# Optimization experiments

Measured on AMD Instinct MI355X. Metric: run time of the kernel, lower is better.

Reference implementation:

```python
import jax, jax.numpy as jnp
import numpy as np

B, T, W, D = 2, 64, 32, 512
H = 8                      # n_heads
N = 64                     # d_state
EXPAND = 2
DIN = EXPAND * D           # 1024 d_inner
R = -(-D // 16)            # dt_rank = ceil(d_model/16) = 32
K = 4                      # d_conv (mamba default)


def setup_inputs():
    key = jax.random.key(0)
    ks = jax.random.split(key, 20)
    s = 0.02
    inp = {
        'x': jax.random.normal(ks[0], (B, T, W, D), jnp.float32),
        'wq': jax.random.normal(ks[1], (D, D), jnp.float32) * s,
        'bq': jnp.zeros((D,), jnp.float32),
        'wk': jax.random.normal(ks[2], (D, D), jnp.float32) * s,
        'bk': jnp.zeros((D,), jnp.float32),
        'wv': jax.random.normal(ks[3], (D, D), jnp.float32) * s,
        'bv': jnp.zeros((D,), jnp.float32),
        'wo': jax.random.normal(ks[4], (D, D), jnp.float32) * s,
        'bo': jnp.zeros((D,), jnp.float32),
        'in_proj_w': jax.random.normal(ks[5], (2 * DIN, D), jnp.float32) * s,
        'conv_w': jax.random.normal(ks[6], (DIN, 1, K), jnp.float32) * 0.2,
        'conv_b': jnp.zeros((DIN,), jnp.float32),
        'x_proj_w': jax.random.normal(ks[7], (R + 2 * N, DIN), jnp.float32) * s,
        'dt_proj_w': jax.random.normal(ks[8], (DIN, R), jnp.float32) * 0.1,
        'dt_proj_b': jnp.full((DIN,), -4.6, jnp.float32),  # ~softplus^-1(0.01)
        'A_log': jnp.log(jnp.broadcast_to(jnp.arange(1, N + 1, dtype=jnp.float32), (DIN, N))),
        'D_param': jnp.ones((DIN,), jnp.float32),
        'out_proj_w': jax.random.normal(ks[9], (D, DIN), jnp.float32) * s,
        'ln_w': jnp.ones((D,), jnp.float32),
        'ln_b': jnp.zeros((D,), jnp.float32),
    }
    return inp


def _attention(xf, wq, bq, wk, bk, wv, bv, wo, bo):
    b, L, d = xf.shape
    e = d // H
    q = (xf @ wq.T + bq).reshape(b, L, H, e)
    k = (xf @ wk.T + bk).reshape(b, L, H, e)
    v = (xf @ wv.T + bv).reshape(b, L, H, e)
    scale = 1.0 / jnp.sqrt(jnp.float32(e))
    scores = jnp.einsum('blhe,bshe->bhls', q, k) * scale
    causal = jnp.tril(jnp.ones((L, L), bool))
    scores = jnp.where(causal, scores, jnp.finfo(scores.dtype).min)
    attn = jax.nn.softmax(scores, axis=-1)  # dropout off (eval mode)
    out = jnp.einsum('bhls,bshe->blhe', attn, v).reshape(b, L, d)
    return out @ wo.T + bo


def _mamba(xf, in_proj_w, conv_w, conv_b, x_proj_w, dt_proj_w, dt_proj_b,
           A_log, D_param, out_proj_w):
    b, L, d = xf.shape
    xz = xf @ in_proj_w.T                 # (B,L,2*DIN)
    x_in, z = jnp.split(xz, 2, axis=-1)
    # causal depthwise conv1d over L
    xc = jnp.transpose(x_in, (0, 2, 1))   # (B,DIN,L)
    xc = jax.lax.conv_general_dilated(
        xc, conv_w, window_strides=(1,), padding=[(K - 1, 0)],
        feature_group_count=DIN, dimension_numbers=('NCH', 'OIH', 'NCH'))
    xc = xc + conv_b[None, :, None]
    u = jax.nn.silu(jnp.transpose(xc, (0, 2, 1)))   # (B,L,DIN)
    dbc = u @ x_proj_w.T                             # (B,L,R+2N)
    dt, Bm, Cm = dbc[..., :R], dbc[..., R:R + N], dbc[..., R + N:]
    dt = jax.nn.softplus(dt @ dt_proj_w.T + dt_proj_b)  # (B,L,DIN)
    A = -jnp.exp(A_log)                                 # (DIN,N)

    def step(h, t):
        dt_t, B_t, C_t, u_t = t  # (b,DIN),(b,N),(b,N),(b,DIN)
        dA = jnp.exp(dt_t[..., None] * A)                       # (b,DIN,N)
        h = dA * h + (dt_t * u_t)[..., None] * B_t[:, None, :]  # (b,DIN,N)
        y = jnp.einsum('bdn,bn->bd', h, C_t)
        return h, y

    h0 = jnp.zeros((b, DIN, N), xf.dtype)
    xs = (jnp.swapaxes(dt, 0, 1), jnp.swapaxes(Bm, 0, 1),
          jnp.swapaxes(Cm, 0, 1), jnp.swapaxes(u, 0, 1))
    _, ys = jax.lax.scan(step, h0, xs)
    y = jnp.swapaxes(ys, 0, 1) + u * D_param   # (B,L,DIN)
    y = y * jax.nn.silu(z)
    return y @ out_proj_w.T


def reference(x, wq, bq, wk, bk, wv, bv, wo, bo, in_proj_w, conv_w, conv_b,
              x_proj_w, dt_proj_w, dt_proj_b, A_log, D_param, out_proj_w,
              ln_w, ln_b):
    b, t, w, d = x.shape
    L = t * w
    xf = x.reshape(b, L, d)
    x_attn = _attention(xf, wq, bq, wk, bk, wv, bv, wo, bo).reshape(b, t, w, d)
    x_mamba = _mamba(xf, in_proj_w, conv_w, conv_b, x_proj_w, dt_proj_w,
                     dt_proj_b, A_log, D_param, out_proj_w).reshape(b, t, w, d)
    h = x + x_attn + x_mamba
    mu = jnp.mean(h, axis=-1, keepdims=True)
    var = jnp.mean(jnp.square(h - mu), axis=-1, keepdims=True)
    return (h - mu) * jax.lax.rsqrt(var + 1e-5) * ln_w + ln_b
```

## Files before the change

kernel.cpp:

```cpp
#include <hip/hip_runtime.h>

typedef __attribute__((ext_vector_type(4))) float f32x4;
typedef __attribute__((ext_vector_type(8))) short short8;
typedef __attribute__((ext_vector_type(2))) unsigned uint2e;

#define DEV static __device__ __forceinline__

DEV ushort f2b(float f) {
  union { float f; unsigned u; } v; v.f = f;
  unsigned r = v.u + 0x7FFF + ((v.u >> 16) & 1);
  return (ushort)(r >> 16);
}
DEV unsigned pack_bf2(float lo, float hi) {
  return (unsigned)f2b(lo) | ((unsigned)f2b(hi) << 16);
}
DEV float bflo(unsigned p) { return __uint_as_float(p << 16); }
DEV float bfhi(unsigned p) { return __uint_as_float(p & 0xFFFF0000u); }
DEV float b2f(ushort u) { return __uint_as_float((unsigned)u << 16); }

DEV float fexp2(float x) { float r; asm("v_exp_f32 %0, %1" : "=v"(r) : "v"(x)); return r; }

DEV float xor32_add_lo(float s) {
  uint2e r = __builtin_amdgcn_permlane32_swap(__float_as_uint(s), __float_as_uint(s), false, false);
  return s + __uint_as_float(r.x);
}

#define QP(x, ctrl) __int_as_float(__builtin_amdgcn_update_dpp(0, __float_as_int(x), (ctrl), 0xf, 0xf, false))
#define SWZ(x, off) __int_as_float(__builtin_amdgcn_ds_swizzle(__float_as_int(x), (off)))
#define DPP_ADD(x, ctrl, rmask) \
  ((x) + __int_as_float(__builtin_amdgcn_update_dpp(0, __float_as_int(x), (ctrl), (rmask), 0xf, false)))

#define LOG2E 1.44269504f

#define BB    2
#define LL    2048
#define DD    512
#define HH    8
#define EE    64
#define DIN   1024
#define NS    64
#define RR    32
#define BL    4096
#define NCH   16
#define TC    128
#define NC    1536
#define NQ    3584
#define XOFF  1536
#define ZOFF  2560
#define MFMA(a,b,c) __builtin_amdgcn_mfma_f32_16x16x32_bf16((a),(b),(c),0,0,0)

struct CvtJobs {
  const float* src[7];
  ushort*      dst[7];
  int          n[7];
};

__global__ __launch_bounds__(256) void cvt_multi(CvtJobs j) {
  int job = blockIdx.y;
  const float* s = j.src[job];
  ushort* d = j.dst[job];
  int n = j.n[job];
  for (int i = blockIdx.x * 256 + threadIdx.x; i < n; i += gridDim.x * 256)
    d[i] = f2b(s[i]);
}

__global__ __launch_bounds__(256) void pack_wcomb(
    const float* __restrict__ wo, const float* __restrict__ opw,
    const float* __restrict__ bq, const float* __restrict__ bk,
    const float* __restrict__ bv, ushort* __restrict__ wc,
    float* __restrict__ bqi)
{
  int i = blockIdx.x * 256 + threadIdx.x;
  if (i < NQ)
    bqi[i] = (i < DD) ? bq[i] : (i < 2 * DD) ? bk[i - DD] : (i < NC) ? bv[i - 2 * DD] : 0.f;
  if (i >= DD * NC) return;
  int n = i / NC, c = i - n * NC;
  float v = (c < DD) ? wo[n * DD + c] : opw[n * DIN + (c - DD)];
  wc[i] = f2b(v);
}

__global__ __launch_bounds__(256) void gemm_bt(
    const ushort* __restrict__ A, const ushort* __restrict__ W,
    const float* __restrict__ bias, float* __restrict__ outF,
    ushort* __restrict__ outB, int M, int N, int K, int act)
{
  __shared__ ushort As[64][40];
  __shared__ ushort Ws[64][40];
  int m0 = blockIdx.y * 64, n0 = blockIdx.x * 64;
  int tid = threadIdx.x, l = tid & 63, w = tid >> 6;
  int wm = (w >> 1) * 32, wn = (w & 1) * 32;
  int lr = l & 15, kl = (l >> 4) * 8;
  int srow = tid >> 2, sk = (tid & 3) * 8;
  f32x4 acc[2][2] = {};

  for (int k0 = 0; k0 < K; k0 += 32) {
    uint4 av = *(const uint4*)&A[(size_t)(m0 + srow) * K + k0 + sk];
    uint4 wv;
    if (n0 + srow < N) wv = *(const uint4*)&W[(size_t)(n0 + srow) * K + k0 + sk];
    else { wv.x = 0; wv.y = 0; wv.z = 0; wv.w = 0; }
    *(uint4*)&As[srow][sk] = av;
    *(uint4*)&Ws[srow][sk] = wv;
    __syncthreads();
    short8 a0 = *(const short8*)&As[wm + lr][kl];
    short8 a1 = *(const short8*)&As[wm + 16 + lr][kl];
    short8 b0 = *(const short8*)&Ws[wn + lr][kl];
    short8 b1 = *(const short8*)&Ws[wn + 16 + lr][kl];
    acc[0][0] = MFMA(a0, b0, acc[0][0]);
    acc[0][1] = MFMA(a0, b1, acc[0][1]);
    acc[1][0] = MFMA(a1, b0, acc[1][0]);
    acc[1][1] = MFMA(a1, b1, acc[1][1]);
    __syncthreads();
  }

  #pragma unroll
  for (int mi = 0; mi < 2; mi++)
    #pragma unroll
    for (int ni = 0; ni < 2; ni++) {
      int rbase = m0 + wm + mi * 16 + ((l >> 4) << 2);
      int col = n0 + wn + ni * 16 + lr;
      if (col < N) {
        float bval = bias ? bias[col] : 0.f;
        #pragma unroll
        for (int r = 0; r < 4; r++) {
          float v = acc[mi][ni][r] + bval;
          if (act == 1) v = (v > 20.f) ? v : log1pf(__expf(v));
          size_t o = (size_t)(rbase + r) * N + col;
          if (outF) outF[o] = v;
          if (outB) outB[o] = f2b(v);
        }
      }
    }
}

__global__ __launch_bounds__(256) void gemm128(
    const ushort* __restrict__ A, const ushort* __restrict__ W,
    const float* __restrict__ bias, float* __restrict__ outF,
    ushort* __restrict__ outB, int M, int N, int K)
{
  __shared__ ushort As[128][40];
  __shared__ ushort Ws[128][40];
  int tid = threadIdx.x, l = tid & 63, w = tid >> 6;
  int m0 = blockIdx.y * 128, n0 = blockIdx.x * 128;
  int wm = (w >> 1) * 64, wn = (w & 1) * 64;
  int lr = l & 15, kl = (l >> 4) * 8;
  int srow = tid >> 1, sk = (tid & 1) * 16;
  f32x4 acc[4][4] = {};

  const ushort* Ap = A + (size_t)(m0 + srow) * K + sk;
  const ushort* Wp = W + (size_t)(n0 + srow) * K + sk;

  for (int k0 = 0; k0 < K; k0 += 32) {
    uint4 a0 = *(const uint4*)(Ap);
    uint4 a1 = *(const uint4*)(Ap + 8);
    uint4 b0 = *(const uint4*)(Wp);
    uint4 b1 = *(const uint4*)(Wp + 8);
    __syncthreads();
    *(uint4*)&As[srow][sk]     = a0;
    *(uint4*)&As[srow][sk + 8] = a1;
    *(uint4*)&Ws[srow][sk]     = b0;
    *(uint4*)&Ws[srow][sk + 8] = b1;
    __syncthreads();
    short8 af[4], bf[4];
    #pragma unroll
    for (int mi = 0; mi < 4; mi++) af[mi] = *(const short8*)&As[wm + mi * 16 + lr][kl];
    #pragma unroll
    for (int ni = 0; ni < 4; ni++) bf[ni] = *(const short8*)&Ws[wn + ni * 16 + lr][kl];
    #pragma unroll
    for (int mi = 0; mi < 4; mi++)
      #pragma unroll
      for (int ni = 0; ni < 4; ni++)
        acc[mi][ni] = MFMA(af[mi], bf[ni], acc[mi][ni]);
    Ap += 32; Wp += 32;
  }

  #pragma unroll
  for (int mi = 0; mi < 4; mi++)
    #pragma unroll
    for (int ni = 0; ni < 4; ni++) {
      int rbase = m0 + wm + mi * 16 + ((l >> 4) << 2);
      int col = n0 + wn + ni * 16 + lr;
      float bval = bias ? bias[col] : 0.f;
      #pragma unroll
      for (int r = 0; r < 4; r++) {
        float v = acc[mi][ni][r] + bval;
        size_t o = (size_t)(rbase + r) * N + col;
        if (outF) outF[o] = v;
        if (outB) outB[o] = f2b(v);
      }
    }
}

__global__ __launch_bounds__(256) void attn_xproj(
    const ushort* __restrict__ qkv, ushort* __restrict__ comb,
    const ushort* __restrict__ ub, const ushort* __restrict__ xpw,
    float* __restrict__ dbc)
{
  __shared__ ushort smem[4 * 64 * 72];
  int id = blockIdx.x;
  int tid = threadIdx.x, l = tid & 63, w = tid >> 6;

  if (id < 512) {
    typedef ushort row72[72];
    row72* Qs = (row72*)smem;
    row72* Ks = Qs + 64;
    row72* Vt = Ks + 64;
    row72* Ps = Vt + 64;
    int qt = 31 - (id & 31), h = (id >> 5) & 7, b = id >> 8;
    int w16 = w * 16, lr = l & 15, kl = (l >> 4) * 8;

    for (int i = tid; i < 512; i += 256) {
      int row = i >> 3, c8 = (i & 7) * 8;
      *(uint4*)&Qs[row][c8] =
          *(const uint4*)&qkv[((size_t)(b * LL + qt * 64 + row)) * NQ + h * EE + c8];
    }
    __syncthreads();

    float l_r[4] = {0.f, 0.f, 0.f, 0.f};
    f32x4 oacc[4] = {};
    const float SSC = 0.125f * LOG2E;

    for (int kv = 0; kv <= qt; kv++) {
      for (int i = tid; i < 512; i += 256) {
        int s = i >> 3, c8 = (i & 7) * 8;
        size_t rb = ((size_t)(b * LL + kv * 64 + s)) * NQ + h * EE + c8;
        *(uint4*)&Ks[s][c8] = *(const uint4*)&qkv[rb + DD];
        uint4 vv = *(const uint4*)&qkv[rb + 2 * DD];
        const ushort* pv = (const ushort*)&vv;
        #pragma unroll
        for (int jj = 0; jj < 8; jj++) Vt[c8 + jj][s] = pv[jj];
      }
      __syncthreads();

      f32x4 sacc[4] = {};
      #pragma unroll
      for (int kk = 0; kk < 2; kk++) {
        short8 aq = *(const short8*)&Qs[w16 + lr][kk * 32 + kl];
        #pragma unroll
        for (int nt = 0; nt < 4; nt++) {
          short8 bk8 = *(const short8*)&Ks[nt * 16 + lr][kk * 32 + kl];
          sacc[nt] = MFMA(aq, bk8, sacc[nt]);
        }
      }

      bool diag = (kv == qt);
      #pragma unroll
      for (int r = 0; r < 4; r++) {
        int rloc = w16 + ((l >> 4) << 2) + r;
        float rs = 0.f;
        #pragma unroll
        for (int nt = 0; nt < 4; nt++) {
          float v = sacc[nt][r] * SSC;
          if (diag && (nt * 16 + lr) > rloc) v = -1e30f;
          float p = fexp2(v);
          rs += p;
          Ps[rloc][nt * 16 + lr] = f2b(p);
        }
        rs += QP(rs, 0xB1);
        rs += QP(rs, 0x4E);
        rs += SWZ(rs, 0x101F);
        rs += SWZ(rs, 0x201F);
        l_r[r] += rs;
      }

      #pragma unroll
      for (int kk = 0; kk < 2; kk++) {
        short8 ap = *(const short8*)&Ps[w16 + lr][kk * 32 + kl];
        #pragma unroll
        for (int nt = 0; nt < 4; nt++) {
          short8 bv8 = *(const short8*)&Vt[nt * 16 + lr][kk * 32 + kl];
          oacc[nt] = MFMA(ap, bv8, oacc[nt]);
        }
      }
      __syncthreads();
    }

    #pragma unroll
    for (int nt = 0; nt < 4; nt++)
      #pragma unroll
      for (int r = 0; r < 4; r++) {
        int row = qt * 64 + w16 + ((l >> 4) << 2) + r;
        float v = oacc[nt][r] / l_r[r];
        comb[((size_t)(b * LL + row)) * NC + h * EE + nt * 16 + lr] = f2b(v);
      }
  } else {
    typedef ushort row40[40];
    row40* As = (row40*)smem;
    row40* Ws = As + 64;
    int rid = id - 512;
    int n0 = (rid % 3) * 64, m0 = (rid / 3) * 64;
    int wm = (w >> 1) * 32, wn = (w & 1) * 32;
    int lr = l & 15, kl = (l >> 4) * 8;
    int srow = tid >> 2, sk = (tid & 3) * 8;
    f32x4 acc[2][2] = {};

    for (int k0 = 0; k0 < DIN; k0 += 32) {
      uint4 av = *(const uint4*)&ub[(size_t)(m0 + srow) * DIN + k0 + sk];
      uint4 wv;
      if (n0 + srow < 160) wv = *(const uint4*)&xpw[(size_t)(n0 + srow) * DIN + k0 + sk];
      else { wv.x = 0; wv.y = 0; wv.z = 0; wv.w = 0; }
      *(uint4*)&As[srow][sk] = av;
      *(uint4*)&Ws[srow][sk] = wv;
      __syncthreads();
      short8 a0 = *(const short8*)&As[wm + lr][kl];
      short8 a1 = *(const short8*)&As[wm + 16 + lr][kl];
      short8 b0 = *(const short8*)&Ws[wn + lr][kl];
      short8 b1 = *(const short8*)&Ws[wn + 16 + lr][kl];
      acc[0][0] = MFMA(a0, b0, acc[0][0]);
      acc[0][1] = MFMA(a0, b1, acc[0][1]);
      acc[1][0] = MFMA(a1, b0, acc[1][0]);
      acc[1][1] = MFMA(a1, b1, acc[1][1]);
      __syncthreads();
    }

    #pragma unroll
    for (int mi = 0; mi < 2; mi++)
      #pragma unroll
      for (int ni = 0; ni < 2; ni++) {
        int rbase = m0 + wm + mi * 16 + ((l >> 4) << 2);
        int col = n0 + wn + ni * 16 + lr;
        if (col < 160) {
          #pragma unroll
          for (int r = 0; r < 4; r++)
            dbc[(size_t)(rbase + r) * 160 + col] = acc[mi][ni][r];
        }
      }
  }
}

__global__ __launch_bounds__(256) void conv_silu(
    const ushort* __restrict__ xz, const float* __restrict__ cw,
    const float* __restrict__ cb, ushort* __restrict__ ub)
{
  int i = blockIdx.x * 256 + threadIdx.x;
  if (i >= BL * DIN) return;
  int d = i & (DIN - 1);
  int bl = i >> 10;
  int t = bl & (LL - 1);
  int b = bl >> 11;
  float s = cb[d];
  #pragma unroll
  for (int j = 0; j < 4; j++) {
    int tt = t - 3 + j;
    if (tt >= 0) s += b2f(xz[((size_t)(b * LL + tt)) * NQ + XOFF + d]) * cw[d * 4 + j];
  }
  float r = s / (1.f + __expf(-s));
  ub[i] = f2b(r);
}

__global__ __launch_bounds__(256) void dt_bc(
    const float* __restrict__ dbc, const ushort* __restrict__ dtw,
    const float* __restrict__ dtb, ushort* __restrict__ dt_b,
    unsigned* __restrict__ bbp, float4* __restrict__ bcp4)
{
  __shared__ ushort As[64][40];
  __shared__ ushort Ws[64][40];
  int id = blockIdx.x;
  int tid = threadIdx.x;
  if (id < 1024) {
    int m0 = (id >> 4) * 64, n0 = (id & 15) * 64;
    int l = tid & 63, w = tid >> 6;
    int wm = (w >> 1) * 32, wn = (w & 1) * 32;
    int lr = l & 15, kl = (l >> 4) * 8;
    int srow = tid >> 2, sk = (tid & 3) * 8;

    const float* ar = dbc + (size_t)(m0 + srow) * 160 + sk;
    short8 av;
    #pragma unroll
    for (int j = 0; j < 8; j++) ((ushort*)&av)[j] = f2b(ar[j]);
    *(short8*)&As[srow][sk] = av;
    *(uint4*)&Ws[srow][sk] = *(const uint4*)&dtw[(size_t)(n0 + srow) * RR + sk];
    __syncthreads();

    f32x4 acc[2][2] = {};
    short8 a0 = *(const short8*)&As[wm + lr][kl];
    short8 a1 = *(const short8*)&As[wm + 16 + lr][kl];
    short8 b0 = *(const short8*)&Ws[wn + lr][kl];
    short8 b1 = *(const short8*)&Ws[wn + 16 + lr][kl];
    acc[0][0] = MFMA(a0, b0, acc[0][0]);
    acc[0][1] = MFMA(a0, b1, acc[0][1]);
    acc[1][0] = MFMA(a1, b0, acc[1][0]);
    acc[1][1] = MFMA(a1, b1, acc[1][1]);

    #pragma unroll
    for (int mi = 0; mi < 2; mi++)
      #pragma unroll
      for (int ni = 0; ni < 2; ni++) {
        int rbase = m0 + wm + mi * 16 + ((l >> 4) << 2);
        int col = n0 + wn + ni * 16 + lr;
        float bval = dtb[col];
        #pragma unroll
        for (int r = 0; r < 4; r++) {
          float v = acc[mi][ni][r] + bval;
          v = (v > 20.f) ? v : log1pf(__expf(v));
          dt_b[(size_t)(rbase + r) * DIN + col] = f2b(v);
        }
      }
  } else {
    int i = (id - 1024) * 256 + tid;
    int n = i & 63, tp = (i >> 6) & 1023, b = i >> 16;
    size_t r0 = ((size_t)(b * LL + 2 * tp)) * 160;
    float B0 = dbc[r0 + 32 + n],  C0 = dbc[r0 + 96 + n];
    float B1 = dbc[r0 + 192 + n], C1 = dbc[r0 + 256 + n];
    bbp[i] = pack_bf2(B0, B1);
    bcp4[i] = make_float4(B0, C0, B1, C1);
  }
}

__global__ __launch_bounds__(256) void pack_dtu(
    const ushort* __restrict__ dtb16, const ushort* __restrict__ ub,
    const ushort* __restrict__ xz, const float* __restrict__ dpar,
    unsigned* __restrict__ dtu_p, unsigned* __restrict__ sg_p)
{
  __shared__ float s_dt[32][65], s_du[32][65], s_gz[32][65], s_ug[32][65];
  int d0 = blockIdx.x * 64, t0 = blockIdx.y * 32;
  int tid = threadIdx.x;
  int c = tid & 63, r4 = tid >> 6;
  float Dv = dpar[d0 + c];
  #pragma unroll
  for (int k = 0; k < 8; k++) {
    int r = k * 4 + r4;
    size_t row = (size_t)(t0 + r);
    float dtv = b2f(dtb16[row * DIN + d0 + c]);
    float uv  = b2f(ub   [row * DIN + d0 + c]);
    float zz  = b2f(xz   [row * NQ + ZOFF + d0 + c]);
    float g = zz / (1.f + __expf(-zz));
    s_dt[r][c] = dtv;
    s_du[r][c] = dtv * uv;
    s_gz[r][c] = g;
    s_ug[r][c] = uv * Dv * g;
  }
  __syncthreads();
  int dl = tid >> 2, q = tid & 3;
  int b = t0 >> 11, tl0 = t0 & (LL - 1);
  size_t obase = ((size_t)(b * DIN + d0 + dl)) * LL + tl0 + q * 8;
  #pragma unroll
  for (int tt = 0; tt < 8; tt++) {
    int t = q * 8 + tt;
    dtu_p[obase + tt] = pack_bf2(s_dt[t][dl], s_du[t][dl]);
    sg_p [obase + tt] = pack_bf2(s_gz[t][dl], s_ug[t][dl]);
  }
}

__global__ __launch_bounds__(256) void scan_phase1(
    const unsigned* __restrict__ dtu_p, const unsigned* __restrict__ bbp,
    const float* __restrict__ alog, float* __restrict__ hf, float* __restrict__ ap)
{
  __shared__ float lds[4][TC][2];
  int tid = threadIdx.x, w = tid >> 6, l = tid & 63;
  int wid = blockIdx.x * 4 + w;
  int d = wid & (DIN - 1);
  int c = (wid >> 10) & (NCH - 1);
  int b = wid >> 14;
  float An2 = -__expf(alog[d * NS + l]) * LOG2E;

  size_t pbase = ((size_t)(b * DIN + d)) * LL + c * TC;
  unsigned p0 = dtu_p[pbase + l];
  unsigned p1 = dtu_p[pbase + 64 + l];
  float s0 = bflo(p0), s1 = bflo(p1);
  s0 = DPP_ADD(s0, 0x111, 0xf); s0 = DPP_ADD(s0, 0x112, 0xf);
  s0 = DPP_ADD(s0, 0x114, 0xf); s0 = DPP_ADD(s0, 0x118, 0xf);
  s0 = DPP_ADD(s0, 0x142, 0xa); s0 = DPP_ADD(s0, 0x143, 0xc);
  s1 = DPP_ADD(s1, 0x111, 0xf); s1 = DPP_ADD(s1, 0x112, 0xf);
  s1 = DPP_ADD(s1, 0x114, 0xf); s1 = DPP_ADD(s1, 0x118, 0xf);
  s1 = DPP_ADD(s1, 0x142, 0xa); s1 = DPP_ADD(s1, 0x143, 0xc);
  float T0 = __uint_as_float(__builtin_amdgcn_readlane(__float_as_uint(s0), 63));
  float T  = T0 + __uint_as_float(__builtin_amdgcn_readlane(__float_as_uint(s1), 63));
  lds[w][l][0]      = T - s0;
  lds[w][l][1]      = bfhi(p0);
  lds[w][64 + l][0] = (T - T0) - s1;
  lds[w][64 + l][1] = bfhi(p1);
  __syncthreads();

  const unsigned* bq = bbp + ((size_t)(b * 1024 + c * 64) * 64 + l);
  float h0 = 0.f, h1 = 0.f;
  for (int g = 0; g < 16; g++) {
    unsigned bv[4];
    #pragma unroll
    for (int k = 0; k < 4; k++) bv[k] = bq[k * 64];
    const float* gb = &lds[w][g * 8][0];
    #pragma unroll
    for (int j = 0; j < 8; j++) {
      float2 dd = *(const float2*)(gb + j * 2);
      float Bv = (j & 1) ? bfhi(bv[j >> 1]) : bflo(bv[j >> 1]);
      float a = fexp2(dd.x * An2);
      if (j & 1) h1 += a * (dd.y * Bv);
      else       h0 += a * (dd.y * Bv);
    }
    bq += 256;
  }
  size_t o = (((size_t)((b << 10) + d) * NCH) + c) * 64 + l;
  hf[o] = h0 + h1;
  ap[o] = fexp2(T * An2);
}

__global__ __launch_bounds__(256) void scan_carry(
    const float* __restrict__ hf, const float* __restrict__ ap,
    float* __restrict__ carry)
{
  int i = blockIdx.x * 256 + threadIdx.x;
  int n = i & 63;
  int d = (i >> 6) & (DIN - 1);
  int b = i >> 16;
  size_t base = ((size_t)((b << 10) + d) * NCH) * 64 + n;
  float cur = 0.f;
  #pragma unroll
  for (int c = 0; c < NCH; c++) {
    carry[base + (size_t)c * 64] = cur;
    cur = ap[base + (size_t)c * 64] * cur + hf[base + (size_t)c * 64];
  }
}

__global__ __launch_bounds__(256) void scan_phase3(
    const unsigned* __restrict__ dtu_p, const unsigned* __restrict__ sg_p,
    const float4* __restrict__ bcp4, const float* __restrict__ alog,
    const float* __restrict__ carry, ushort* __restrict__ ymt)
{
  __shared__ float lds[4][TC][4];
  __shared__ ushort yt[4][TC];
  int tid = threadIdx.x, w = tid >> 6, l = tid & 63;
  int wid = blockIdx.x * 4 + w;
  int d = wid & (DIN - 1);
  int c = (wid >> 10) & (NCH - 1);
  int b = wid >> 14;
  float An2 = -__expf(alog[d * NS + l]) * LOG2E;

  size_t pbase = ((size_t)(b * DIN + d)) * LL + c * TC;
  #pragma unroll
  for (int q = 0; q < 2; q++) {
    unsigned pd = dtu_p[pbase + q * 64 + l];
    unsigned pg = sg_p [pbase + q * 64 + l];
    lds[w][q * 64 + l][0] = bflo(pd);
    lds[w][q * 64 + l][1] = bfhi(pd);
    lds[w][q * 64 + l][2] = bflo(pg);
    lds[w][q * 64 + l][3] = bfhi(pg);
  }
  __syncthreads();

  float h = carry[(((size_t)((b << 10) + d) * NCH) + c) * 64 + l];
  const float4* bq = bcp4 + ((size_t)(b * 1024 + c * 64) * 64 + l);
  bool s1f = l & 1, s2f = l & 2, s4f = l & 4;
  bool wl = l < 8;

  for (int g = 0; g < 16; g++) {
    float4 bcs[4];
    bcs[0] = bq[0]; bcs[1] = bq[64]; bcs[2] = bq[128]; bcs[3] = bq[192];
    const float* gb = &lds[w][g * 8][0];
    float p[8];
    #pragma unroll
    for (int j = 0; j < 8; j++) {
      float2 dd = *(const float2*)(gb + j * 4);
      float Bv = (j & 1) ? bcs[j >> 1].z : bcs[j >> 1].x;
      float Cv = (j & 1) ? bcs[j >> 1].w : bcs[j >> 1].y;
      float a = fexp2(dd.x * An2);
      h = a * h + dd.y * Bv;
      p[j] = h * Cv;
    }
    #pragma unroll
    for (int j = 0; j < 8; j++) p[j] += QP(p[j], 0xB1);
    float q0 = s1f ? p[1] : p[0];
    float q1 = s1f ? p[3] : p[2];
    float q2 = s1f ? p[5] : p[4];
    float q3 = s1f ? p[7] : p[6];
    q0 += QP(q0, 0x4E); q1 += QP(q1, 0x4E);
    q2 += QP(q2, 0x4E); q3 += QP(q3, 0x4E);
    float r0 = s2f ? q1 : q0;
    float r1 = s2f ? q3 : q2;
    r0 += SWZ(r0, 0x101F); r1 += SWZ(r1, 0x101F);
    float s = s4f ? r1 : r0;
    s += QP(s, 0x128);
    s += SWZ(s, 0x401F);
    s = xor32_add_lo(s);

    float2 sgv = *(const float2*)(&lds[w][g * 8 + (l & 7)][2]);
    if (wl) yt[w][g * 8 + l] = f2b(s * sgv.x + sgv.y);
    bq += 256;
  }
  __syncthreads();
  unsigned vv = *(const unsigned*)&yt[w][2 * l];
  ((unsigned*)(ymt + pbase))[l] = vv;
}

__global__ __launch_bounds__(256) void transpose_ym(
    const ushort* __restrict__ ymt, ushort* __restrict__ comb)
{
  __shared__ ushort tile[64][72];
  int tid = threadIdx.x;
  int bx = blockIdx.x;
  int by = blockIdx.y;
  int b  = blockIdx.z;
  int r = tid >> 2, c16 = (tid & 3) * 16;
  const ushort* src = ymt + ((size_t)(b * DIN + bx * 64 + r)) * LL + by * 64 + c16;
  *(uint4*)&tile[r][c16]     = *(const uint4*)src;
  *(uint4*)&tile[r][c16 + 8] = *(const uint4*)(src + 8);
  __syncthreads();
  ushort tmp[16];
  #pragma unroll
  for (int j = 0; j < 16; j++) tmp[j] = tile[c16 + j][r];
  ushort* dst = comb + ((size_t)(b * LL + by * 64 + r)) * NC + DD + bx * 64 + c16;
  *(uint4*)dst       = *(uint4*)&tmp[0];
  *(uint4*)(dst + 8) = *(uint4*)&tmp[8];
}

__global__ __launch_bounds__(256) void residual_ln(
    const float* __restrict__ x, const float* __restrict__ so,
    const float* __restrict__ lw, const float* __restrict__ lb,
    float* __restrict__ out)
{
  int row = blockIdx.x * 4 + (threadIdx.x >> 6);
  int l = threadIdx.x & 63;
  size_t base = (size_t)row * DD;
  float h[8];
  float s = 0.f, s2 = 0.f;
  #pragma unroll
  for (int half = 0; half < 2; half++) {
    int c = half * 256 + l * 4;
    float4 xv = *(const float4*)(x + base + c);
    float4 sv = *(const float4*)(so + base + c);
    float* hp = h + half * 4;
    hp[0] = xv.x + sv.x;
    hp[1] = xv.y + sv.y;
    hp[2] = xv.z + sv.z;
    hp[3] = xv.w + sv.w;
    #pragma unroll
    for (int j = 0; j < 4; j++) { s += hp[j]; s2 += hp[j] * hp[j]; }
  }
  #pragma unroll
  for (int o = 1; o < 64; o <<= 1) { s += __shfl_xor(s, o); s2 += __shfl_xor(s2, o); }
  float mean = s * (1.f / DD);
  float var = s2 * (1.f / DD) - mean * mean;
  float rs = rsqrtf(var + 1e-5f);
  #pragma unroll
  for (int half = 0; half < 2; half++) {
    int c = half * 256 + l * 4;
    float4 ov;
    ov.x = (h[half*4+0] - mean) * rs * lw[c+0] + lb[c+0];
    ov.y = (h[half*4+1] - mean) * rs * lw[c+1] + lb[c+1];
    ov.z = (h[half*4+2] - mean) * rs * lw[c+2] + lb[c+2];
    ov.w = (h[half*4+3] - mean) * rs * lw[c+3] + lb[c+3];
    *(float4*)(out + base + c) = ov;
  }
}

extern "C" void kernel_launch(void* const* d_in, const int* in_sizes, int n_in,
                              void* d_out, int out_size, void* d_ws, size_t ws_size,
                              hipStream_t stream) {
  const float* x    = (const float*)d_in[0];
  const float* wq   = (const float*)d_in[1];
  const float* bq   = (const float*)d_in[2];
  const float* wk   = (const float*)d_in[3];
  const float* bk   = (const float*)d_in[4];
  const float* wv   = (const float*)d_in[5];
  const float* bv   = (const float*)d_in[6];
  const float* wo   = (const float*)d_in[7];
  const float* bo   = (const float*)d_in[8];
  const float* inw  = (const float*)d_in[9];
  const float* cw   = (const float*)d_in[10];
  const float* cb   = (const float*)d_in[11];
  const float* xpw  = (const float*)d_in[12];
  const float* dtw  = (const float*)d_in[13];
  const float* dtb  = (const float*)d_in[14];
  const float* alog = (const float*)d_in[15];
  const float* dpar = (const float*)d_in[16];
  const float* opw  = (const float*)d_in[17];
  const float* lnw  = (const float*)d_in[18];
  const float* lnb  = (const float*)d_in[19];

  char* ws = (char*)d_ws;
  size_t off = 0;
  auto alloc = [&](size_t bytes) -> void* {
    void* p = ws + off;
    off += (bytes + 255) & ~(size_t)255;
    return p;
  };

  const size_t BLD = (size_t)BL * DD;
  const size_t BLDIN = (size_t)BL * DIN;

  ushort* xf_b   = (ushort*)alloc(BLD * 2);
  ushort* wqi_b  = (ushort*)alloc((size_t)NQ * DD * 2);
  float*  bqi    = (float*)alloc(NQ * 4);
  ushort* xpw_b  = (ushort*)alloc(160 * DIN * 2);
  ushort* dtw_b  = (ushort*)alloc(DIN * RR * 2);
  ushort* wcomb_b= (ushort*)alloc((size_t)DD * NC * 2);
  ushort* qkvxz_b= (ushort*)alloc((size_t)BL * NQ * 2);
  ushort* comb_a = (ushort*)alloc((size_t)BL * NC * 2);
  float*  sum_o  = (float*)alloc(BLD * 4);
  ushort* u_b    = (ushort*)alloc(BLDIN * 2);
  float*  dbc    = (float*)alloc((size_t)BL * 160 * 4);
  ushort* dt_b   = (ushort*)alloc(BLDIN * 2);
  ushort* ymt_b  = (ushort*)alloc(BLDIN * 2);
  unsigned* bbp  = (unsigned*)alloc((size_t)BB * (LL / 2) * NS * 4);
  float4* bcp4   = (float4*)alloc((size_t)BB * (LL / 2) * NS * sizeof(float4));
  unsigned* dtu_p = (unsigned*)alloc(BLDIN * 4);
  unsigned* sg_p  = (unsigned*)alloc(BLDIN * 4);

  const size_t SCN = (size_t)BB * DIN * NCH * 64;
  float* hf_s    = (float*)qkvxz_b;
  float* ap_s    = hf_s + SCN;
  float* carry_s = (float*)alloc(SCN * 4);

  CvtJobs cj;
  cj.src[0] = x;    cj.dst[0] = xf_b;                cj.n[0] = (int)BLD;
  cj.src[1] = wq;   cj.dst[1] = wqi_b;               cj.n[1] = DD * DD;
  cj.src[2] = wk;   cj.dst[2] = wqi_b + DD * DD;     cj.n[2] = DD * DD;
  cj.src[3] = wv;   cj.dst[3] = wqi_b + 2 * DD * DD; cj.n[3] = DD * DD;
  cj.src[4] = inw;  cj.dst[4] = wqi_b + 3 * DD * DD; cj.n[4] = 2 * DIN * DD;
  cj.src[5] = xpw;  cj.dst[5] = xpw_b;               cj.n[5] = 160 * DIN;
  cj.src[6] = dtw;  cj.dst[6] = dtw_b;               cj.n[6] = DIN * RR;
  cvt_multi<<<dim3(256, 7), 256, 0, stream>>>(cj);
  pack_wcomb<<<dim3((DD * NC + 255) / 256), 256, 0, stream>>>(wo, opw, bq, bk, bv, wcomb_b, bqi);

  gemm128<<<dim3(28, 32), 256, 0, stream>>>(xf_b, wqi_b, bqi, nullptr, qkvxz_b, BL, NQ, DD);

  conv_silu<<<dim3(32768), 256, 0, stream>>>(qkvxz_b, cw, cb, u_b);

  attn_xproj<<<dim3(704), 256, 0, stream>>>(qkvxz_b, comb_a, u_b, xpw_b, dbc);

  dt_bc<<<dim3(1536), 256, 0, stream>>>(dbc, dtw_b, dtb, dt_b, bbp, bcp4);

  pack_dtu<<<dim3(16, 128), 256, 0, stream>>>(dt_b, u_b, qkvxz_b, dpar, dtu_p, sg_p);
  scan_phase1<<<dim3(8192), 256, 0, stream>>>(dtu_p, bbp, alog, hf_s, ap_s);
  scan_carry<<<dim3(512), 256, 0, stream>>>(hf_s, ap_s, carry_s);
  scan_phase3<<<dim3(8192), 256, 0, stream>>>(dtu_p, sg_p, bcp4, alog, carry_s, ymt_b);
  transpose_ym<<<dim3(16, 32, BB), 256, 0, stream>>>(ymt_b, comb_a);

  gemm_bt<<<dim3(8, 64), 256, 0, stream>>>(comb_a, wcomb_b, bo, sum_o, nullptr, BL, DD, NC, 0);

  residual_ln<<<dim3(1024), 256, 0, stream>>>(x, sum_o, lnw, lnb, (float*)d_out);
}
```

Before: 364.5 us.

## Fuse chunked scan phases into one block per channel and register-tile conv

New measurement: 379.7 us. 1.04x slower.

```diff
diff --git a/kernel.cpp b/kernel.cpp
--- a/kernel.cpp
+++ b/kernel.cpp
@@ -332,19 +332,27 @@
     const float* __restrict__ cb, ushort* __restrict__ ub)
 {
   int i = blockIdx.x * 256 + threadIdx.x;
-  if (i >= BL * DIN) return;
   int d = i & (DIN - 1);
-  int bl = i >> 10;
-  int t = bl & (LL - 1);
-  int b = bl >> 11;
-  float s = cb[d];
-  #pragma unroll
-  for (int j = 0; j < 4; j++) {
-    int tt = t - 3 + j;
-    if (tt >= 0) s += b2f(xz[((size_t)(b * LL + tt)) * NQ + XOFF + d]) * cw[d * 4 + j];
-  }
-  float r = s / (1.f + __expf(-s));
-  ub[i] = f2b(r);
+  int r = i >> 10;
+  int t0 = (r & (LL / 8 - 1)) * 8;
+  int b = r >> 8;
+  float c0 = cw[d * 4], c1 = cw[d * 4 + 1], c2 = cw[d * 4 + 2], c3 = cw[d * 4 + 3];
+  float bias = cb[d];
+  float xw[11];
+  #pragma unroll
+  for (int j = 0; j < 3; j++) {
+    int tt = t0 - 3 + j;
+    xw[j] = (tt >= 0) ? b2f(xz[((size_t)(b * LL + tt)) * NQ + XOFF + d]) : 0.f;
+  }
+  #pragma unroll
+  for (int j = 0; j < 8; j++)
+    xw[3 + j] = b2f(xz[((size_t)(b * LL + t0 + j)) * NQ + XOFF + d]);
+  size_t obase = (size_t)(b * LL + t0) * DIN + d;
+  #pragma unroll
+  for (int j = 0; j < 8; j++) {
+    float s = bias + xw[j] * c0 + xw[j + 1] * c1 + xw[j + 2] * c2 + xw[j + 3] * c3;
+    ub[obase + (size_t)j * DIN] = f2b(s / (1.f + __expf(-s)));
+  }
 }
 
 __global__ __launch_bounds__(256) void dt_bc(
@@ -441,16 +449,20 @@
   }
 }
 
-__global__ __launch_bounds__(256) void scan_phase1(
-    const unsigned* __restrict__ dtu_p, const unsigned* __restrict__ bbp,
-    const float* __restrict__ alog, float* __restrict__ hf, float* __restrict__ ap)
-{
-  __shared__ float lds[4][TC][2];
+__global__ __launch_bounds__(1024) void scan_fused(
+    const unsigned* __restrict__ dtu_p, const unsigned* __restrict__ sg_p,
+    const unsigned* __restrict__ bbp, const float4* __restrict__ bcp4,
+    const float* __restrict__ alog, ushort* __restrict__ ymt)
+{
+  __shared__ float lds3[NCH][TC][4];
+  __shared__ float hfL[NCH][NS];
+  __shared__ float apL[NCH][NS];
+  __shared__ ushort yt[NCH][TC];
   int tid = threadIdx.x, w = tid >> 6, l = tid & 63;
-  int wid = blockIdx.x * 4 + w;
-  int d = wid & (DIN - 1);
-  int c = (wid >> 10) & (NCH - 1);
-  int b = wid >> 14;
+  int bid = blockIdx.x;
+  int d = bid & (DIN - 1);
+  int b = bid >> 10;
+  int c = w;
   float An2 = -__expf(alog[d * NS + l]) * LOG2E;
 
   size_t pbase = ((size_t)(b * DIN + d)) * LL + c * TC;
@@ -465,86 +477,60 @@
   s1 = DPP_ADD(s1, 0x142, 0xa); s1 = DPP_ADD(s1, 0x143, 0xc);
   float T0 = __uint_as_float(__builtin_amdgcn_readlane(__float_as_uint(s0), 63));
   float T  = T0 + __uint_as_float(__builtin_amdgcn_readlane(__float_as_uint(s1), 63));
-  lds[w][l][0]      = T - s0;
-  lds[w][l][1]      = bfhi(p0);
-  lds[w][64 + l][0] = (T - T0) - s1;
-  lds[w][64 + l][1] = bfhi(p1);
+  lds3[w][l][0]      = T - s0;
+  lds3[w][l][1]      = bfhi(p0);
+  lds3[w][64 + l][0] = (T - T0) - s1;
+  lds3[w][64 + l][1] = bfhi(p1);
   __syncthreads();
 
-  const unsigned* bq = bbp + ((size_t)(b * 1024 + c * 64) * 64 + l);
-  float h0 = 0.f, h1 = 0.f;
-  for (int g = 0; g < 16; g++) {
-    unsigned bv[4];
-    #pragma unroll
-    for (int k = 0; k < 4; k++) bv[k] = bq[k * 64];
-    const float* gb = &lds[w][g * 8][0];
-    #pragma unroll
-    for (int j = 0; j < 8; j++) {
-      float2 dd = *(const float2*)(gb + j * 2);
-      float Bv = (j & 1) ? bfhi(bv[j >> 1]) : bflo(bv[j >> 1]);
-      float a = fexp2(dd.x * An2);
-      if (j & 1) h1 += a * (dd.y * Bv);
-      else       h0 += a * (dd.y * Bv);
+  {
+    const unsigned* bq = bbp + ((size_t)(b * 1024 + c * 64) * 64 + l);
+    float h0 = 0.f, h1 = 0.f;
+    for (int g = 0; g < 16; g++) {
+      unsigned bv[4];
+      #pragma unroll
+      for (int k = 0; k < 4; k++) bv[k] = bq[k * 64];
+      const float* gb = &lds3[w][g * 8][0];
+      #pragma unroll
+      for (int j = 0; j < 8; j++) {
+        float2 dd = *(const float2*)(gb + j * 4);
+        float Bv = (j & 1) ? bfhi(bv[j >> 1]) : bflo(bv[j >> 1]);
+        float a = fexp2(dd.x * An2);
+        if (j & 1) h1 += a * (dd.y * Bv);
+        else       h0 += a * (dd.y * Bv);
+      }
+      bq += 256;
     }
-    bq += 256;
-  }
-  size_t o = (((size_t)((b << 10) + d) * NCH) + c) * 64 + l;
-  hf[o] = h0 + h1;
-  ap[o] = fexp2(T * An2);
-}
-
-__global__ __launch_bounds__(256) void scan_carry(
-    const float* __restrict__ hf, const float* __restrict__ ap,
-    float* __restrict__ carry)
-{
-  int i = blockIdx.x * 256 + threadIdx.x;
-  int n = i & 63;
-  int d = (i >> 6) & (DIN - 1);
-  int b = i >> 16;
-  size_t base = ((size_t)((b << 10) + d) * NCH) * 64 + n;
-  float cur = 0.f;
-  #pragma unroll
-  for (int c = 0; c < NCH; c++) {
-    carry[base + (size_t)c * 64] = cur;
-    cur = ap[base + (size_t)c * 64] * cur + hf[base + (size_t)c * 64];
-  }
-}
-
-__global__ __launch_bounds__(256) void scan_phase3(
-    const unsigned* __restrict__ dtu_p, const unsigned* __restrict__ sg_p,
-    const float4* __restrict__ bcp4, const float* __restrict__ alog,
-    const float* __restrict__ carry, ushort* __restrict__ ymt)
-{
-  __shared__ float lds[4][TC][4];
-  __shared__ ushort yt[4][TC];
-  int tid = threadIdx.x, w = tid >> 6, l = tid & 63;
-  int wid = blockIdx.x * 4 + w;
-  int d = wid & (DIN - 1);
-  int c = (wid >> 10) & (NCH - 1);
-  int b = wid >> 14;
-  float An2 = -__expf(alog[d * NS + l]) * LOG2E;
-
-  size_t pbase = ((size_t)(b * DIN + d)) * LL + c * TC;
-  #pragma unroll
-  for (int q = 0; q < 2; q++) {
-    unsigned pd = dtu_p[pbase + q * 64 + l];
-    unsigned pg = sg_p [pbase + q * 64 + l];
-    lds[w][q * 64 + l][0] = bflo(pd);
-    lds[w][q * 64 + l][1] = bfhi(pd);
-    lds[w][q * 64 + l][2] = bflo(pg);
-    lds[w][q * 64 + l][3] = bfhi(pg);
+    hfL[w][l] = h0 + h1;
+    apL[w][l] = fexp2(T * An2);
   }
   __syncthreads();
 
-  float h = carry[(((size_t)((b << 10) + d) * NCH) + c) * 64 + l];
-  const float4* bq = bcp4 + ((size_t)(b * 1024 + c * 64) * 64 + l);
+  float h = 0.f;
+  for (int k = 0; k < c; k++) h = apL[k][l] * h + hfL[k][l];
+
+  {
+    unsigned pg0 = sg_p[pbase + l];
+    unsigned pg1 = sg_p[pbase + 64 + l];
+    lds3[w][l][0]      = bflo(p0);
+    lds3[w][l][1]      = bfhi(p0);
+    lds3[w][l][2]      = bflo(pg0);
+    lds3[w][l][3]      = bfhi(pg0);
+    lds3[w][64 + l][0] = bflo(p1);
+    lds3[w][64 + l][1] = bfhi(p1);
+    lds3[w][64 + l][2] = bflo(pg1);
+    lds3[w][64 + l][3] = bfhi(pg1);
+  }
+  __syncthreads();
+
+  const float4* bq4 = bcp4 + ((size_t)(b * 1024 + c * 64) * 64 + l);
   bool s1f = l & 1, s2f = l & 2, s4f = l & 4;
   bool wl = l < 8;
 
   for (int g = 0; g < 16; g++) {
     float4 bcs[4];
-    bcs[0] = bq[0]; bcs[1] = bq[64]; bcs[2] = bq[128]; bcs[3] = bq[192];
-    const float* gb = &lds[w][g * 8][0];
+    bcs[0] = bq4[0]; bcs[1] = bq4[64]; bcs[2] = bq4[128]; bcs[3] = bq4[192];
+    const float* gb = &lds3[w][g * 8][0];
     float p[8];
     #pragma unroll
     for (int j = 0; j < 8; j++) {
@@ -571,9 +557,9 @@
     s += SWZ(s, 0x401F);
     s = xor32_add_lo(s);
 
-    float2 sgv = *(const float2*)(&lds[w][g * 8 + (l & 7)][2]);
+    float2 sgv = *(const float2*)(&lds3[w][g * 8 + (l & 7)][2]);
     if (wl) yt[w][g * 8 + l] = f2b(s * sgv.x + sgv.y);
-    bq += 256;
+    bq4 += 256;
   }
   __syncthreads();
   unsigned vv = *(const unsigned*)&yt[w][2 * l];
@@ -694,11 +680,6 @@
   unsigned* dtu_p = (unsigned*)alloc(BLDIN * 4);
   unsigned* sg_p  = (unsigned*)alloc(BLDIN * 4);
 
-  const size_t SCN = (size_t)BB * DIN * NCH * 64;
-  float* hf_s    = (float*)qkvxz_b;
-  float* ap_s    = hf_s + SCN;
-  float* carry_s = (float*)alloc(SCN * 4);
-
   CvtJobs cj;
   cj.src[0] = x;    cj.dst[0] = xf_b;                cj.n[0] = (int)BLD;
   cj.src[1] = wq;   cj.dst[1] = wqi_b;               cj.n[1] = DD * DD;
@@ -712,16 +693,14 @@
 
   gemm128<<<dim3(28, 32), 256, 0, stream>>>(xf_b, wqi_b, bqi, nullptr, qkvxz_b, BL, NQ, DD);
 
-  conv_silu<<<dim3(32768), 256, 0, stream>>>(qkvxz_b, cw, cb, u_b);
+  conv_silu<<<dim3(2048), 256, 0, stream>>>(qkvxz_b, cw, cb, u_b);
 
   attn_xproj<<<dim3(704), 256, 0, stream>>>(qkvxz_b, comb_a, u_b, xpw_b, dbc);
 
   dt_bc<<<dim3(1536), 256, 0, stream>>>(dbc, dtw_b, dtb, dt_b, bbp, bcp4);
 
   pack_dtu<<<dim3(16, 128), 256, 0, stream>>>(dt_b, u_b, qkvxz_b, dpar, dtu_p, sg_p);
-  scan_phase1<<<dim3(8192), 256, 0, stream>>>(dtu_p, bbp, alog, hf_s, ap_s);
-  scan_carry<<<dim3(512), 256, 0, stream>>>(hf_s, ap_s, carry_s);
-  scan_phase3<<<dim3(8192), 256, 0, stream>>>(dtu_p, sg_p, bcp4, alog, carry_s, ymt_b);
+  scan_fused<<<dim3(BB * DIN), 1024, 0, stream>>>(dtu_p, sg_p, bbp, bcp4, alog, ymt_b);
   transpose_ym<<<dim3(16, 32, BB), 256, 0, stream>>>(ymt_b, comb_a);
 
   gemm_bt<<<dim3(8, 64), 256, 0, stream>>>(comb_a, wcomb_b, bo, sum_o, nullptr, BL, DD, NC, 0);
```
